# Kernel tuning notes

Hardware: AMD Instinct MI355X
Metric: run time of the kernel (lower is better)

The kernel has to match this reference:

```python
import jax, jax.numpy as jnp
import numpy as np
import math

E = 512      # embed_dim
H = 8        # num_heads
D = E // H   # head_embed_dim
B = 1
S = 4096

def setup_inputs() -> dict:
    key = jax.random.key(0)
    ks = jax.random.split(key, 9)
    s = 1.0 / math.sqrt(E)
    return {
        "Q": jax.random.normal(ks[0], (B, S, E), dtype=jnp.float32),
        "K": jax.random.normal(ks[1], (B, S, E), dtype=jnp.float32),
        "V": jax.random.normal(ks[2], (B, S, E), dtype=jnp.float32),
        "W_qk": jax.random.uniform(ks[3], (E, E), jnp.float32, -s, s),
        "b_qk": jax.random.uniform(ks[4], (E,), jnp.float32, -s, s),
        "W_v": jax.random.uniform(ks[5], (E, E), jnp.float32, -s, s),
        "b_v": jax.random.uniform(ks[6], (E,), jnp.float32, -s, s),
        "W_out": jax.random.uniform(ks[7], (E, E), jnp.float32, -s, s),
        "b_out": jax.random.uniform(ks[8], (E,), jnp.float32, -s, s),
    }

def reference(Q, K, V, W_qk, b_qk, W_v, b_v, W_out, b_out):
    # shared qk projection (torch Linear: x @ W.T + b)
    q = Q @ W_qk.T + b_qk
    k = K @ W_qk.T + b_qk
    v = V @ W_v.T + b_v
    # NOTE: original uses .view(B, H, S, D) -- a pure reshape, no transpose
    q = q.reshape(B, H, S, D)
    k = k.reshape(B, H, S, D)
    v = v.reshape(B, H, S, D)
    scores = jnp.einsum("bhsd,bhtd->bhst", q, k) / math.sqrt(D)
    attn = jax.nn.softmax(scores, axis=-1)
    out = jnp.einsum("bhst,bhtd->bhsd", attn, v)
    out = out.reshape(B, S, E)  # matches .view merge
    return out @ W_out.T + b_out
```

## Files before the change

### kernel.cpp

```cpp
#include <hip/hip_runtime.h>
#include <hip/hip_bf16.h>
#include <math.h>

typedef __hip_bfloat16 hbf16;
typedef __attribute__((ext_vector_type(4))) float f32x4;
typedef __attribute__((ext_vector_type(8))) __bf16 bf16x8;
typedef __attribute__((ext_vector_type(4))) short short4v;

#define MFMA16(a, b, c) __builtin_amdgcn_mfma_f32_16x16x32_bf16((a), (b), (c), 0, 0, 0)

#if __has_builtin(__builtin_amdgcn_mfma_f32_16x16x16bf16_1k)
#define MFMA16K16(a, b, c) __builtin_amdgcn_mfma_f32_16x16x16bf16_1k((a), (b), (c), 0, 0, 0)
#else
__device__ __forceinline__ f32x4 mfma16k16_asm(short4v a, short4v b, f32x4 c) {
  asm("v_mfma_f32_16x16x16_bf16 %0, %1, %2, %0" : "+v"(c) : "v"(a), "v"(b));
  return c;
}
#define MFMA16K16(a, b, c) mfma16k16_asm((a), (b), (c))
#endif

__device__ __forceinline__ void gload_lds16(const hbf16* g, hbf16* l) {
  __builtin_amdgcn_global_load_lds(
      (const __attribute__((address_space(1))) void*)g,
      (__attribute__((address_space(3))) void*)l, 16, 0, 0);
}

__device__ __forceinline__ void cvt4(const float* __restrict__ s, hbf16* __restrict__ d, int i) {
  float4 v = reinterpret_cast<const float4*>(s)[i];
  union { hbf16 h[4]; uint2 u; } pk;
  pk.h[0] = __float2bfloat16(v.x);
  pk.h[1] = __float2bfloat16(v.y);
  pk.h[2] = __float2bfloat16(v.z);
  pk.h[3] = __float2bfloat16(v.w);
  reinterpret_cast<uint2*>(d)[i] = pk.u;
}

__global__ __launch_bounds__(256) void cvt_all_kernel(
    const float* __restrict__ Q, const float* __restrict__ K, const float* __restrict__ V,
    const float* __restrict__ Wqk, const float* __restrict__ Wv, const float* __restrict__ Wout,
    hbf16* __restrict__ Qb, hbf16* __restrict__ Kb, hbf16* __restrict__ Vb,
    hbf16* __restrict__ Wqkb, hbf16* __restrict__ Wvb, hbf16* __restrict__ Woutb,
    int n4big, int n4w) {
  int stride = gridDim.x * blockDim.x;
  for (int i = blockIdx.x * blockDim.x + threadIdx.x; i < n4big; i += stride) {
    cvt4(Q, Qb, i);
    cvt4(K, Kb, i);
    cvt4(V, Vb, i);
    if (i < n4w) {
      cvt4(Wqk, Wqkb, i);
      cvt4(Wv, Wvb, i);
      cvt4(Wout, Woutb, i);
    }
  }
}

__device__ __forceinline__ void stage_a64(const hbf16* __restrict__ A, int K, int bm, int k0,
                                          hbf16* Alds, int wave, int lane) {
  const int row = wave * 16 + (lane >> 2);
  gload_lds16(A + (size_t)(bm * 64 + row) * K + k0 + (lane & 3) * 8, Alds + wave * 512);
}
__device__ __forceinline__ void stage_b128(const hbf16* __restrict__ B, int K, int bn, int k0,
                                           hbf16* Blds, int wave, int lane) {
#pragma unroll
  for (int i = 0; i < 2; ++i) {
    const int row = wave * 32 + i * 16 + (lane >> 2);
    gload_lds16(B + (size_t)(bn * 128 + row) * K + k0 + (lane & 3) * 8,
                Blds + wave * 1024 + i * 512);
  }
}

__device__ __forceinline__ void gemm_core_2ph(
    const hbf16* __restrict__ A, const hbf16* __restrict__ B, int K, int bm, int bn,
    hbf16* Alds , hbf16* Blds , f32x4 (&acc)[4][2]) {
  const int tid = threadIdx.x;
  const int lane = tid & 63;
  const int wave = tid >> 6;
  const int l15 = lane & 15, lg = lane >> 4;
  const int nt = K >> 5;
  stage_a64(A, K, bm, 0, Alds, wave, lane);
  stage_b128(B, K, bn, 0, Blds, wave, lane);
  __syncthreads();
  int cur = 0;
  for (int t = 0; t < nt; ++t) {
    if (t + 1 < nt) {
      stage_a64(A, K, bm, (t + 1) * 32, Alds + (cur ^ 1) * 2048, wave, lane);
      stage_b128(B, K, bn, (t + 1) * 32, Blds + (cur ^ 1) * 4096, wave, lane);
    }
    bf16x8 af[4], bfv[2];
#pragma unroll
    for (int m = 0; m < 4; ++m)
      af[m] = *reinterpret_cast<const bf16x8*>(&Alds[cur * 2048 + (m * 16 + l15) * 32 + lg * 8]);
#pragma unroll
    for (int n = 0; n < 2; ++n)
      bfv[n] = *reinterpret_cast<const bf16x8*>(
          &Blds[cur * 4096 + (wave * 32 + n * 16 + l15) * 32 + lg * 8]);
#pragma unroll
    for (int m = 0; m < 4; ++m)
#pragma unroll
      for (int n = 0; n < 2; ++n)
        acc[m][n] = MFMA16(af[m], bfv[n], acc[m][n]);
    __syncthreads();
    cur ^= 1;
  }
}

__global__ __launch_bounds__(256) void proj_fused_kernel(
    const hbf16* __restrict__ Qb, const hbf16* __restrict__ Kb, const hbf16* __restrict__ Vb,
    const hbf16* __restrict__ Wqk, const hbf16* __restrict__ Wv,
    const float* __restrict__ bqk, const float* __restrict__ bv,
    hbf16* __restrict__ qp, hbf16* __restrict__ kp, hbf16* __restrict__ vT) {
  __shared__ __align__(16) hbf16 Alds[2 * 2048];
  __shared__ __align__(16) hbf16 Blds[2 * 4096];
  const int z = blockIdx.y;
  const int lane = threadIdx.x & 63, wave = threadIdx.x >> 6;
  const int l15 = lane & 15, lg = lane >> 4;

  f32x4 acc[4][2];
  const f32x4 zero = {0.f, 0.f, 0.f, 0.f};
#pragma unroll
  for (int m = 0; m < 4; ++m)
#pragma unroll
    for (int n = 0; n < 2; ++n) acc[m][n] = zero;

  if (z < 2) {
    const hbf16* A = z ? Kb : Qb;
    hbf16* outp = z ? kp : qp;
    const int bm = blockIdx.x & 63, bn = blockIdx.x >> 6;
    gemm_core_2ph(A, Wqk, 512, bm, bn, Alds, Blds, acc);
    const float qscale = z ? 1.0f : 0.125f * 1.4426950408889634f;
    const int row0 = bm * 64;
    const int col0 = bn * 128 + wave * 32;
#pragma unroll
    for (int m = 0; m < 4; ++m) {
#pragma unroll
      for (int n = 0; n < 2; ++n) {
        const int col = col0 + n * 16 + l15;
        const float bsv = bqk[col];
#pragma unroll
        for (int j = 0; j < 4; ++j) {
          const int row = row0 + m * 16 + lg * 4 + j;
          outp[(size_t)row * 512 + col] = __float2bfloat16((acc[m][n][j] + bsv) * qscale);
        }
      }
    }
  } else {
    const int bm = blockIdx.x >> 5;
    const int bn = blockIdx.x & 31;
    gemm_core_2ph(Wv, Vb, 512, bm, bn, Alds, Blds, acc);
    const int row0 = bm * 64;
    const int col0 = bn * 128 + wave * 32;
#pragma unroll
    for (int m = 0; m < 4; ++m) {
#pragma unroll
      for (int n = 0; n < 2; ++n) {
        const int col = col0 + n * 16 + l15;
#pragma unroll
        for (int j = 0; j < 4; ++j) {
          const int row = row0 + m * 16 + lg * 4 + j;
          const int h = col >> 9;
          const int p = ((col & 511) << 3) + (row >> 6);
          const int d = row & 63;
          vT[(size_t)h * 262144 + (size_t)d * 4096 + p] =
              __float2bfloat16(acc[m][n][j] + bv[row]);
        }
      }
    }
  }
}

__global__ __launch_bounds__(256) void out_gemm_kernel(
    const hbf16* __restrict__ A, const hbf16* __restrict__ B, const float* __restrict__ bias,
    float* __restrict__ out) {
  __shared__ __align__(16) hbf16 Alds[2 * 2048];
  __shared__ __align__(16) hbf16 Blds[2 * 4096];
  const int bm = blockIdx.x & 63, bn = blockIdx.x >> 6;
  const int lane = threadIdx.x & 63, wave = threadIdx.x >> 6;
  const int l15 = lane & 15, lg = lane >> 4;
  f32x4 acc[4][2];
  const f32x4 zero = {0.f, 0.f, 0.f, 0.f};
#pragma unroll
  for (int m = 0; m < 4; ++m)
#pragma unroll
    for (int n = 0; n < 2; ++n) acc[m][n] = zero;

  gemm_core_2ph(A, B, 512, bm, bn, Alds, Blds, acc);

  const int row0 = bm * 64;
  const int col0 = bn * 128 + wave * 32;
#pragma unroll
  for (int m = 0; m < 4; ++m) {
#pragma unroll
    for (int n = 0; n < 2; ++n) {
      const int col = col0 + n * 16 + l15;
      const float bsv = bias[col];
#pragma unroll
      for (int j = 0; j < 4; ++j) {
        const int row = row0 + m * 16 + lg * 4 + j;
        out[(size_t)row * 512 + col] = acc[m][n][j] + bsv;
      }
    }
  }
}

__device__ __forceinline__ void stage64(const hbf16* __restrict__ g, int gstride,
                                        hbf16* tile, int wave, int lane) {
#pragma unroll
  for (int ii = 0; ii < 2; ++ii) {
    const int i = wave * 2 + ii;
    const int row = i * 8 + (lane >> 3);
    const int ce = ((lane & 7) ^ (lane >> 3)) << 3;
    gload_lds16(g + (size_t)row * gstride + ce, tile + i * 512);
  }
}

template <bool DIRECT>
__global__ __launch_bounds__(256, 4) void attn_kernel4(
    const hbf16* __restrict__ qp, const hbf16* __restrict__ kp,
    const hbf16* __restrict__ vT, hbf16* __restrict__ ao,
    float* __restrict__ Opart, float* __restrict__ Lpart,
    int kv_per_split, int nwg) {
  const int lin = blockIdx.x + 32 * (blockIdx.y + 8 * blockIdx.z);
  const int chunk = nwg >> 3;
  const int swz = (lin & 7) * chunk + (lin >> 3);
  const int qt = swz & 31;
  const int h = (swz >> 5) & 7;
  const int split = swz >> 8;

  const hbf16* qh = qp + (size_t)h * 262144;
  const hbf16* kh = kp + (size_t)h * 262144;
  const hbf16* vh = vT + (size_t)h * 262144;

  const int lane = threadIdx.x & 63, wave = threadIdx.x >> 6;
  const int l15 = lane & 15, lg = lane >> 4;
  const int qrow0 = qt * 128 + wave * 32;
  const int kv0 = split * kv_per_split;
  const int nkt = kv_per_split >> 6;

  __shared__ __align__(16) hbf16 Kt[2][4096];
  __shared__ __align__(16) hbf16 Vt[2][4096];

  bf16x8 qf[2][2];
#pragma unroll
  for (int rb = 0; rb < 2; ++rb)
#pragma unroll
    for (int dc = 0; dc < 2; ++dc)
      qf[rb][dc] = *reinterpret_cast<const bf16x8*>(
          &qh[(size_t)(qrow0 + rb * 16 + l15) * 64 + dc * 32 + lg * 8]);

  float lsum[2] = {0.f, 0.f};
  f32x4 oaccT[2][4];
  const f32x4 zero = {0.f, 0.f, 0.f, 0.f};
#pragma unroll
  for (int rb = 0; rb < 2; ++rb)
#pragma unroll
    for (int db = 0; db < 4; ++db) oaccT[rb][db] = zero;

  stage64(kh + (size_t)kv0 * 64, 64, Kt[0], wave, lane);
  stage64(vh + kv0, 4096, Vt[0], wave, lane);
  __syncthreads();

  int cur = 0;
  for (int t = 0; t < nkt; ++t) {
    if (t + 1 < nkt) {
      const int kb = kv0 + (t + 1) * 64;
      stage64(kh + (size_t)kb * 64, 64, Kt[cur ^ 1], wave, lane);
      stage64(vh + kb, 4096, Vt[cur ^ 1], wave, lane);
    }
    const hbf16* Kc = Kt[cur];
    const hbf16* Vc = Vt[cur];

    f32x4 s[2][4];
#pragma unroll
    for (int rb = 0; rb < 2; ++rb)
#pragma unroll
      for (int cb = 0; cb < 4; ++cb) s[rb][cb] = zero;
#pragma unroll
    for (int cb = 0; cb < 4; ++cb) {
      const int krow = cb * 16 + l15;
      const int sw = l15 & 7;
#pragma unroll
      for (int dc = 0; dc < 2; ++dc) {
        bf16x8 kf = *reinterpret_cast<const bf16x8*>(
            &Kc[krow * 64 + (((dc * 4 + lg) ^ sw) << 3)]);
#pragma unroll
        for (int rb = 0; rb < 2; ++rb) s[rb][cb] = MFMA16(kf, qf[rb][dc], s[rb][cb]);
      }
    }

    short4v pb[2][4];
#pragma unroll
    for (int rb = 0; rb < 2; ++rb)
#pragma unroll
      for (int cb = 0; cb < 4; ++cb) {
        const float p0 = exp2f(s[rb][cb][0]);
        const float p1 = exp2f(s[rb][cb][1]);
        const float p2 = exp2f(s[rb][cb][2]);
        const float p3 = exp2f(s[rb][cb][3]);
        lsum[rb] += (p0 + p1) + (p2 + p3);
        union { hbf16 h[4]; short4v v; } pk;
        pk.h[0] = __float2bfloat16(p0);
        pk.h[1] = __float2bfloat16(p1);
        pk.h[2] = __float2bfloat16(p2);
        pk.h[3] = __float2bfloat16(p3);
        pb[rb][cb] = pk.v;
      }

#pragma unroll
    for (int db = 0; db < 4; ++db) {
      const int d = db * 16 + l15;
      const int swd = d & 7;
#pragma unroll
      for (int cb = 0; cb < 4; ++cb) {
        short4v vf = *reinterpret_cast<const short4v*>(
            &Vc[d * 64 + (((2 * cb + (lg >> 1)) ^ swd) << 3) + ((lg & 1) << 2)]);
#pragma unroll
        for (int rb = 0; rb < 2; ++rb)
          oaccT[rb][db] = MFMA16K16(vf, pb[rb][cb], oaccT[rb][db]);
      }
    }
    __syncthreads();
    cur ^= 1;
  }

#pragma unroll
  for (int rb = 0; rb < 2; ++rb) {
    lsum[rb] += __shfl_xor(lsum[rb], 16);
    lsum[rb] += __shfl_xor(lsum[rb], 32);
  }
  if (DIRECT) {
    hbf16* oh = ao + (size_t)h * 262144;
#pragma unroll
    for (int rb = 0; rb < 2; ++rb) {
      const float inv = 1.f / lsum[rb];
      const int row = qrow0 + rb * 16 + l15;
#pragma unroll
      for (int db = 0; db < 4; ++db) {
        union { hbf16 h[4]; uint2 u; } pk;
#pragma unroll
        for (int j = 0; j < 4; ++j) pk.h[j] = __float2bfloat16(oaccT[rb][db][j] * inv);
        *reinterpret_cast<uint2*>(&oh[(size_t)row * 64 + db * 16 + lg * 4]) = pk.u;
      }
    }
  } else {
    const size_t hrow0 = (size_t)split * 32768 + (size_t)h * 4096;
#pragma unroll
    for (int rb = 0; rb < 2; ++rb) {
      const int row = qrow0 + rb * 16 + l15;
#pragma unroll
      for (int db = 0; db < 4; ++db) {
        float4 v;
        v.x = oaccT[rb][db][0]; v.y = oaccT[rb][db][1];
        v.z = oaccT[rb][db][2]; v.w = oaccT[rb][db][3];
        *reinterpret_cast<float4*>(&Opart[(hrow0 + row) * 64 + db * 16 + lg * 4]) = v;
      }
      if (lg == 0) Lpart[hrow0 + row] = lsum[rb];
    }
  }
}

__global__ __launch_bounds__(256) void attn_combine_kernel(
    const float* __restrict__ Opart, const float* __restrict__ Lpart,
    hbf16* __restrict__ ao, int splits) {
  const int t = threadIdx.x;
  const int hrow = blockIdx.x * 64 + (t >> 2);
  const int d0 = (t & 3) * 16;
  float denom = 0.f;
  for (int s = 0; s < splits; ++s) denom += Lpart[s * 32768 + hrow];
  const float inv = 1.f / denom;
  float4 acc[4] = {};
  for (int s = 0; s < splits; ++s) {
    const float4* p = reinterpret_cast<const float4*>(
        Opart + ((size_t)s * 32768 + hrow) * 64 + d0);
#pragma unroll
    for (int i = 0; i < 4; ++i) {
      float4 v = p[i];
      acc[i].x += v.x; acc[i].y += v.y; acc[i].z += v.z; acc[i].w += v.w;
    }
  }
  union { hbf16 h[16]; uint4 u[2]; } pk;
#pragma unroll
  for (int i = 0; i < 4; ++i) {
    pk.h[i * 4 + 0] = __float2bfloat16(acc[i].x * inv);
    pk.h[i * 4 + 1] = __float2bfloat16(acc[i].y * inv);
    pk.h[i * 4 + 2] = __float2bfloat16(acc[i].z * inv);
    pk.h[i * 4 + 3] = __float2bfloat16(acc[i].w * inv);
  }
  uint4* dst = reinterpret_cast<uint4*>(ao + (size_t)hrow * 64 + d0);
  dst[0] = pk.u[0];
  dst[1] = pk.u[1];
}

extern "C" void kernel_launch(void* const* d_in, const int* in_sizes, int n_in,
                              void* d_out, int out_size, void* d_ws, size_t ws_size,
                              hipStream_t stream) {
  const float* Q = (const float*)d_in[0];
  const float* K = (const float*)d_in[1];
  const float* V = (const float*)d_in[2];
  const float* Wqk = (const float*)d_in[3];
  const float* bqk = (const float*)d_in[4];
  const float* Wv = (const float*)d_in[5];
  const float* bv = (const float*)d_in[6];
  const float* Wout = (const float*)d_in[7];
  const float* bout = (const float*)d_in[8];
  float* out = (float*)d_out;

  const size_t NE = (size_t)4096 * 512;
  const size_t WE = (size_t)512 * 512;
  hbf16* ws = (hbf16*)d_ws;
  hbf16* Qb = ws;
  hbf16* Kb = Qb + NE;
  hbf16* Vb = Kb + NE;
  hbf16* Wqkb = Vb + NE;
  hbf16* Wvb = Wqkb + WE;
  hbf16* Woutb = Wvb + WE;
  hbf16* qp = Woutb + WE;
  hbf16* kp = qp + NE;
  hbf16* vT = kp + NE;
  hbf16* ao = vT + NE;

  const size_t base_bytes = (((size_t)(7 * NE + 3 * WE) * 2) + 255) & ~(size_t)255;
  const size_t per_split_bytes = ((size_t)32768 * 64 + 32768) * 4;
  int splits = 1;
  if (ws_size >= base_bytes + 8 * per_split_bytes) splits = 8;
  else if (ws_size >= base_bytes + 4 * per_split_bytes) splits = 4;
  else if (ws_size >= base_bytes + 2 * per_split_bytes) splits = 2;
  float* Opart = (float*)((char*)d_ws + base_bytes);
  float* Lpart = Opart + (size_t)splits * 32768 * 64;

  cvt_all_kernel<<<2048, 256, 0, stream>>>(Q, K, V, Wqk, Wv, Wout,
                                           Qb, Kb, Vb, Wqkb, Wvb, Woutb,
                                           (int)(NE / 4), (int)(WE / 4));
  proj_fused_kernel<<<dim3(256, 3), 256, 0, stream>>>(Qb, Kb, Vb, Wqkb, Wvb, bqk, bv,
                                                      qp, kp, vT);
  if (splits == 1) {
    attn_kernel4<true><<<dim3(32, 8, 1), 256, 0, stream>>>(
        qp, kp, vT, ao, nullptr, nullptr, 4096, 256);
  } else {
    attn_kernel4<false><<<dim3(32, 8, splits), 256, 0, stream>>>(
        qp, kp, vT, nullptr, Opart, Lpart, 4096 / splits, 256 * splits);
    attn_combine_kernel<<<512, 256, 0, stream>>>(Opart, Lpart, ao, splits);
  }
  out_gemm_kernel<<<256, 256, 0, stream>>>(ao, Woutb, bout, out);
}
```

Baseline: 187.1 us.

## Fuse fp32-to-bf16 conversion into GEMM tile loading and drop convert kernel

Removes the separate conversion kernel that wrote bf16 copies of Q, K, V and the weights. The projection and output GEMMs now load fp32 tiles into registers, convert them to bf16, and store them into LDS inside the double-buffered loop. This avoids a full extra read/write pass over the inputs and one launch, but replaces the async global-to-LDS loads with register-staged loads and re-reads the fp32 weights once per tile. The split count for the attention kernel is also capped at 4 instead of 8.

```diff
diff --git a/kernel.cpp b/kernel.cpp
--- a/kernel.cpp
+++ b/kernel.cpp
@@ -25,66 +25,49 @@
       (__attribute__((address_space(3))) void*)l, 16, 0, 0);
 }
 
-__device__ __forceinline__ void cvt4(const float* __restrict__ s, hbf16* __restrict__ d, int i) {
-  float4 v = reinterpret_cast<const float4*>(s)[i];
-  union { hbf16 h[4]; uint2 u; } pk;
-  pk.h[0] = __float2bfloat16(v.x);
-  pk.h[1] = __float2bfloat16(v.y);
-  pk.h[2] = __float2bfloat16(v.z);
-  pk.h[3] = __float2bfloat16(v.w);
-  reinterpret_cast<uint2*>(d)[i] = pk.u;
-}
-
-__global__ __launch_bounds__(256) void cvt_all_kernel(
-    const float* __restrict__ Q, const float* __restrict__ K, const float* __restrict__ V,
-    const float* __restrict__ Wqk, const float* __restrict__ Wv, const float* __restrict__ Wout,
-    hbf16* __restrict__ Qb, hbf16* __restrict__ Kb, hbf16* __restrict__ Vb,
-    hbf16* __restrict__ Wqkb, hbf16* __restrict__ Wvb, hbf16* __restrict__ Woutb,
-    int n4big, int n4w) {
-  int stride = gridDim.x * blockDim.x;
-  for (int i = blockIdx.x * blockDim.x + threadIdx.x; i < n4big; i += stride) {
-    cvt4(Q, Qb, i);
-    cvt4(K, Kb, i);
-    cvt4(V, Vb, i);
-    if (i < n4w) {
-      cvt4(Wqk, Wqkb, i);
-      cvt4(Wv, Wvb, i);
-      cvt4(Wout, Woutb, i);
-    }
-  }
-}
-
-__device__ __forceinline__ void stage_a64(const hbf16* __restrict__ A, int K, int bm, int k0,
-                                          hbf16* Alds, int wave, int lane) {
-  const int row = wave * 16 + (lane >> 2);
-  gload_lds16(A + (size_t)(bm * 64 + row) * K + k0 + (lane & 3) * 8, Alds + wave * 512);
-}
-__device__ __forceinline__ void stage_b128(const hbf16* __restrict__ B, int K, int bn, int k0,
-                                           hbf16* Blds, int wave, int lane) {
-#pragma unroll
-  for (int i = 0; i < 2; ++i) {
-    const int row = wave * 32 + i * 16 + (lane >> 2);
-    gload_lds16(B + (size_t)(bn * 128 + row) * K + k0 + (lane & 3) * 8,
-                Blds + wave * 1024 + i * 512);
-  }
-}
-
-__device__ __forceinline__ void gemm_core_2ph(
-    const hbf16* __restrict__ A, const hbf16* __restrict__ B, int K, int bm, int bn,
+struct F8 { float4 x, y; };
+__device__ __forceinline__ F8 load8(const float* p) {
+  F8 r;
+  r.x = *reinterpret_cast<const float4*>(p);
+  r.y = *reinterpret_cast<const float4*>(p + 4);
+  return r;
+}
+__device__ __forceinline__ uint4 cvt8(const F8& f) {
+  union { hbf16 h[8]; uint4 u; } pk;
+  pk.h[0] = __float2bfloat16(f.x.x); pk.h[1] = __float2bfloat16(f.x.y);
+  pk.h[2] = __float2bfloat16(f.x.z); pk.h[3] = __float2bfloat16(f.x.w);
+  pk.h[4] = __float2bfloat16(f.y.x); pk.h[5] = __float2bfloat16(f.y.y);
+  pk.h[6] = __float2bfloat16(f.y.z); pk.h[7] = __float2bfloat16(f.y.w);
+  return pk.u;
+}
+
+
+__device__ __forceinline__ void gemm2ph_ff(
+    const float* __restrict__ A, const float* __restrict__ B, int K, int bm, int bn,
     hbf16* Alds , hbf16* Blds , f32x4 (&acc)[4][2]) {
   const int tid = threadIdx.x;
-  const int lane = tid & 63;
-  const int wave = tid >> 6;
+  const int lane = tid & 63, wave = tid >> 6;
   const int l15 = lane & 15, lg = lane >> 4;
+  const int arow = tid >> 2, ac = (tid & 3) * 8;
+  const float* Ab = A + (size_t)(bm * 64 + arow) * K + ac;
+  const float* Bb0 = B + (size_t)(bn * 128 + arow) * K + ac;
+  const float* Bb1 = B + (size_t)(bn * 128 + 64 + arow) * K + ac;
+  const int lofs = arow * 32 + ac;
   const int nt = K >> 5;
-  stage_a64(A, K, bm, 0, Alds, wave, lane);
-  stage_b128(B, K, bn, 0, Blds, wave, lane);
+
+  F8 ra = load8(Ab), rb0 = load8(Bb0), rb1 = load8(Bb1);
+  *reinterpret_cast<uint4*>(&Alds[lofs]) = cvt8(ra);
+  *reinterpret_cast<uint4*>(&Blds[lofs]) = cvt8(rb0);
+  *reinterpret_cast<uint4*>(&Blds[2048 + lofs]) = cvt8(rb1);
   __syncthreads();
+
   int cur = 0;
   for (int t = 0; t < nt; ++t) {
+    F8 na, nb0, nb1;
     if (t + 1 < nt) {
-      stage_a64(A, K, bm, (t + 1) * 32, Alds + (cur ^ 1) * 2048, wave, lane);
-      stage_b128(B, K, bn, (t + 1) * 32, Blds + (cur ^ 1) * 4096, wave, lane);
+      na = load8(Ab + (t + 1) * 32);
+      nb0 = load8(Bb0 + (t + 1) * 32);
+      nb1 = load8(Bb1 + (t + 1) * 32);
     }
     bf16x8 af[4], bfv[2];
 #pragma unroll
@@ -99,14 +82,76 @@
 #pragma unroll
       for (int n = 0; n < 2; ++n)
         acc[m][n] = MFMA16(af[m], bfv[n], acc[m][n]);
+    if (t + 1 < nt) {
+      hbf16* Ad = Alds + (cur ^ 1) * 2048;
+      hbf16* Bd = Blds + (cur ^ 1) * 4096;
+      *reinterpret_cast<uint4*>(&Ad[lofs]) = cvt8(na);
+      *reinterpret_cast<uint4*>(&Bd[lofs]) = cvt8(nb0);
+      *reinterpret_cast<uint4*>(&Bd[2048 + lofs]) = cvt8(nb1);
+    }
     __syncthreads();
     cur ^= 1;
   }
 }
 
+__device__ __forceinline__ void stage_a64_bf(const hbf16* __restrict__ A, int K, int bm, int k0,
+                                             hbf16* Alds, int wave, int lane) {
+  const int row = wave * 16 + (lane >> 2);
+  gload_lds16(A + (size_t)(bm * 64 + row) * K + k0 + (lane & 3) * 8, Alds + wave * 512);
+}
+
+__device__ __forceinline__ void gemm2ph_bf(
+    const hbf16* __restrict__ A, const float* __restrict__ B, int K, int bm, int bn,
+    hbf16* Alds, hbf16* Blds, f32x4 (&acc)[4][2]) {
+  const int tid = threadIdx.x;
+  const int lane = tid & 63, wave = tid >> 6;
+  const int l15 = lane & 15, lg = lane >> 4;
+  const int arow = tid >> 2, ac = (tid & 3) * 8;
+  const float* Bb0 = B + (size_t)(bn * 128 + arow) * K + ac;
+  const float* Bb1 = B + (size_t)(bn * 128 + 64 + arow) * K + ac;
+  const int lofs = arow * 32 + ac;
+  const int nt = K >> 5;
+
+  stage_a64_bf(A, K, bm, 0, Alds, wave, lane);
+  F8 rb0 = load8(Bb0), rb1 = load8(Bb1);
+  *reinterpret_cast<uint4*>(&Blds[lofs]) = cvt8(rb0);
+  *reinterpret_cast<uint4*>(&Blds[2048 + lofs]) = cvt8(rb1);
+  __syncthreads();
+
+  int cur = 0;
+  for (int t = 0; t < nt; ++t) {
+    F8 nb0, nb1;
+    if (t + 1 < nt) {
+      stage_a64_bf(A, K, bm, (t + 1) * 32, Alds + (cur ^ 1) * 2048, wave, lane);
+      nb0 = load8(Bb0 + (t + 1) * 32);
+      nb1 = load8(Bb1 + (t + 1) * 32);
+    }
+    bf16x8 af[4], bfv[2];
+#pragma unroll
+    for (int m = 0; m < 4; ++m)
+      af[m] = *reinterpret_cast<const bf16x8*>(&Alds[cur * 2048 + (m * 16 + l15) * 32 + lg * 8]);
+#pragma unroll
+    for (int n = 0; n < 2; ++n)
+      bfv[n] = *reinterpret_cast<const bf16x8*>(
+          &Blds[cur * 4096 + (wave * 32 + n * 16 + l15) * 32 + lg * 8]);
+#pragma unroll
+    for (int m = 0; m < 4; ++m)
+#pragma unroll
+      for (int n = 0; n < 2; ++n)
+        acc[m][n] = MFMA16(af[m], bfv[n], acc[m][n]);
+    if (t + 1 < nt) {
+      hbf16* Bd = Blds + (cur ^ 1) * 4096;
+      *reinterpret_cast<uint4*>(&Bd[lofs]) = cvt8(nb0);
+      *reinterpret_cast<uint4*>(&Bd[2048 + lofs]) = cvt8(nb1);
+    }
+    __syncthreads();
+    cur ^= 1;
+  }
+}
+
 __global__ __launch_bounds__(256) void proj_fused_kernel(
-    const hbf16* __restrict__ Qb, const hbf16* __restrict__ Kb, const hbf16* __restrict__ Vb,
-    const hbf16* __restrict__ Wqk, const hbf16* __restrict__ Wv,
+    const float* __restrict__ Q, const float* __restrict__ K, const float* __restrict__ V,
+    const float* __restrict__ Wqk, const float* __restrict__ Wv,
     const float* __restrict__ bqk, const float* __restrict__ bv,
     hbf16* __restrict__ qp, hbf16* __restrict__ kp, hbf16* __restrict__ vT) {
   __shared__ __align__(16) hbf16 Alds[2 * 2048];
@@ -123,10 +168,10 @@
     for (int n = 0; n < 2; ++n) acc[m][n] = zero;
 
   if (z < 2) {
-    const hbf16* A = z ? Kb : Qb;
+    const float* A = z ? K : Q;
     hbf16* outp = z ? kp : qp;
     const int bm = blockIdx.x & 63, bn = blockIdx.x >> 6;
-    gemm_core_2ph(A, Wqk, 512, bm, bn, Alds, Blds, acc);
+    gemm2ph_ff(A, Wqk, 512, bm, bn, Alds, Blds, acc);
     const float qscale = z ? 1.0f : 0.125f * 1.4426950408889634f;
     const int row0 = bm * 64;
     const int col0 = bn * 128 + wave * 32;
@@ -146,7 +191,7 @@
   } else {
     const int bm = blockIdx.x >> 5;
     const int bn = blockIdx.x & 31;
-    gemm_core_2ph(Wv, Vb, 512, bm, bn, Alds, Blds, acc);
+    gemm2ph_ff(Wv, V, 512, bm, bn, Alds, Blds, acc);
     const int row0 = bm * 64;
     const int col0 = bn * 128 + wave * 32;
 #pragma unroll
@@ -169,7 +214,7 @@
 }
 
 __global__ __launch_bounds__(256) void out_gemm_kernel(
-    const hbf16* __restrict__ A, const hbf16* __restrict__ B, const float* __restrict__ bias,
+    const hbf16* __restrict__ A, const float* __restrict__ B, const float* __restrict__ bias,
     float* __restrict__ out) {
   __shared__ __align__(16) hbf16 Alds[2 * 2048];
   __shared__ __align__(16) hbf16 Blds[2 * 4096];
@@ -183,7 +228,7 @@
 #pragma unroll
     for (int n = 0; n < 2; ++n) acc[m][n] = zero;
 
-  gemm_core_2ph(A, B, 512, bm, bn, Alds, Blds, acc);
+  gemm2ph_bf(A, B, 512, bm, bn, Alds, Blds, acc);
 
   const int row0 = bm * 64;
   const int col0 = bn * 128 + wave * 32;
@@ -405,32 +450,21 @@
   float* out = (float*)d_out;
 
   const size_t NE = (size_t)4096 * 512;
-  const size_t WE = (size_t)512 * 512;
   hbf16* ws = (hbf16*)d_ws;
-  hbf16* Qb = ws;
-  hbf16* Kb = Qb + NE;
-  hbf16* Vb = Kb + NE;
-  hbf16* Wqkb = Vb + NE;
-  hbf16* Wvb = Wqkb + WE;
-  hbf16* Woutb = Wvb + WE;
-  hbf16* qp = Woutb + WE;
+  hbf16* qp = ws;
   hbf16* kp = qp + NE;
   hbf16* vT = kp + NE;
   hbf16* ao = vT + NE;
 
-  const size_t base_bytes = (((size_t)(7 * NE + 3 * WE) * 2) + 255) & ~(size_t)255;
+  const size_t base_bytes = ((4 * NE * 2) + 255) & ~(size_t)255;
   const size_t per_split_bytes = ((size_t)32768 * 64 + 32768) * 4;
   int splits = 1;
-  if (ws_size >= base_bytes + 8 * per_split_bytes) splits = 8;
-  else if (ws_size >= base_bytes + 4 * per_split_bytes) splits = 4;
+  if (ws_size >= base_bytes + 4 * per_split_bytes) splits = 4;
   else if (ws_size >= base_bytes + 2 * per_split_bytes) splits = 2;
   float* Opart = (float*)((char*)d_ws + base_bytes);
   float* Lpart = Opart + (size_t)splits * 32768 * 64;
 
-  cvt_all_kernel<<<2048, 256, 0, stream>>>(Q, K, V, Wqk, Wv, Wout,
-                                           Qb, Kb, Vb, Wqkb, Wvb, Woutb,
-                                           (int)(NE / 4), (int)(WE / 4));
-  proj_fused_kernel<<<dim3(256, 3), 256, 0, stream>>>(Qb, Kb, Vb, Wqkb, Wvb, bqk, bv,
+  proj_fused_kernel<<<dim3(256, 3), 256, 0, stream>>>(Q, K, V, Wqk, Wv, bqk, bv,
                                                       qp, kp, vT);
   if (splits == 1) {
     attn_kernel4<true><<<dim3(32, 8, 1), 256, 0, stream>>>(
@@ -440,5 +474,5 @@
         qp, kp, vT, nullptr, Opart, Lpart, 4096 / splits, 256 * splits);
     attn_combine_kernel<<<512, 256, 0, stream>>>(Opart, Lpart, ao, splits);
   }
-  out_gemm_kernel<<<256, 256, 0, stream>>>(ao, Woutb, bout, out);
-}
+  out_gemm_kernel<<<256, 256, 0, stream>>>(ao, Wout, bout, out);
+}
```

Result: faster. 180.6 us (-3.5%).
